# Optimization experiments

Hardware: AMD Instinct MI355X
Metric: run time of the kernel (lower is better)

## Reference

```python
import jax, jax.numpy as jnp
import numpy as np

N = 100000   # num nodes
E = 1600000  # num edges
D = 128      # input_dim
K = 5        # APPNP propagation steps
EPS = 1e-8   # torch cosine_similarity eps


def setup_inputs() -> dict:
    key = jax.random.key(0)
    k1, k2, k3, k4 = jax.random.split(key, 4)
    x = jax.random.normal(k1, (N, D), jnp.float32)
    mask = jax.random.normal(k2, (N, 1), jnp.float32)
    edge_index = jax.random.randint(k3, (2, E), 0, N, dtype=jnp.int32)
    # init_t: orthogonal weight with gain sqrt(2), zero bias
    W = jax.nn.initializers.orthogonal(scale=2 ** 0.5)(k4, (D, D), jnp.float32)
    b = jnp.zeros((D,), jnp.float32)
    alpha = jnp.array(0.5, jnp.float32)
    return {"x": x, "mask": mask, "edge_index": edge_index, "W": W, "b": b, "alpha": alpha}


def reference(x, mask, edge_index, W, b, alpha):
    n = x.shape[0]
    # x_fn: Linear + Tanh
    h = jnp.tanh(x @ W.T + b)
    src, dst = edge_index[0], edge_index[1]
    hs, hd = h[src], h[dst]  # [E, D] gathers
    # torch F.cosine_similarity with eps-clamped norms
    dot = jnp.sum(hs * hd, axis=-1)
    ns = jnp.maximum(jnp.sqrt(jnp.sum(hs * hs, axis=-1)), EPS)
    nd = jnp.maximum(jnp.sqrt(jnp.sum(hd * hd, axis=-1)), EPS)
    edge_weights = jax.nn.relu(dot / (ns * nd))  # [E]

    fill = jax.nn.relu(mask)  # [N, 1]

    # PyG APPNP: gcn_norm with self loops (fill value 1.0)
    loops = jnp.arange(n, dtype=src.dtype)
    row = jnp.concatenate([src, loops])
    col = jnp.concatenate([dst, loops])
    w = jnp.concatenate([edge_weights, jnp.ones((n,), edge_weights.dtype)])
    deg = jax.ops.segment_sum(w, col, num_segments=n)
    dinv = jnp.where(deg > 0, jax.lax.rsqrt(jnp.maximum(deg, EPS)), 0.0)
    norm = dinv[row] * w * dinv[col]  # [E+N]

    # K-step APPNP: z <- (1-alpha) * A_hat z + alpha * fill
    z = fill
    for _ in range(K):
        agg = jax.ops.segment_sum(norm[:, None] * z[row], col, num_segments=n)
        z = (1.0 - alpha) * agg + alpha * fill
    return z, edge_weights
```

## Files before the change

kernel.cpp:

```cpp
#include <hip/hip_runtime.h>
#include <hip/hip_bf16.h>

typedef __attribute__((ext_vector_type(2))) float f32x2;
typedef __attribute__((ext_vector_type(4))) float f32x4;
typedef __attribute__((ext_vector_type(8))) short short8;

#define D 128
#define EPS 1e-8f
#define BSH 8
#define BSZ 256
#define SMAX 8000
#define OSH 12
#define OBK 4096

__device__ __forceinline__ unsigned int pkbf(float lo, float hi) {
    unsigned int r;
    asm("v_cvt_pk_bf16_f32 %0, %1, %2" : "=v"(r) : "v"(lo), "v"(hi));
    return r;
}

__device__ __forceinline__ float ftanh(float y) {
    float e = __builtin_amdgcn_exp2f(y * 2.885390082f);
    float r = __builtin_amdgcn_rcpf(e + 1.0f);
    return __builtin_fmaf(-2.0f, r, 1.0f);
}

__device__ __forceinline__ int dot4(unsigned int a, unsigned int b, int c) {
#if __has_builtin(__builtin_amdgcn_sdot4)
    return __builtin_amdgcn_sdot4((int)a, (int)b, c, false);
#else
    int r = c;
    r += (int)(char)(a) * (int)(char)(b);
    r += (int)(char)(a >> 8) * (int)(char)(b >> 8);
    r += (int)(char)(a >> 16) * (int)(char)(b >> 16);
    r += (int)(char)(a >> 24) * (int)(char)(b >> 24);
    return r;
#endif
}

__global__ __launch_bounds__(256) void k1_gemm_aux(const float* __restrict__ x,
                                                   const float* __restrict__ W,
                                                   const float* __restrict__ b,
                                                   signed char* __restrict__ hn8,
                                                   int N,
                                                   const float* __restrict__ mask,
                                                   float* __restrict__ fill,
                                                   const int* __restrict__ dst,
                                                   int* __restrict__ M,
                                                   int E, int nbk, int nblk, int chunk,
                                                   int gemmNB) {
    __shared__ char Wlds[D * D * 2];
    int tid = threadIdx.x;

    if (blockIdx.x >= gemmNB) {
        int baux = blockIdx.x - gemmNB;
        int* cnt = (int*)Wlds;
        for (int k = tid; k < nbk; k += 256) cnt[k] = 0;
        int fi = baux * 256 + tid;
        if (fi < N) fill[fi] = fmaxf(mask[fi], 0.0f);
        __syncthreads();
        int beg = baux * chunk, end = min(E, beg + chunk);
        for (int e = beg + tid; e < end; e += 256)
            atomicAdd(&cnt[dst[e] >> BSH], 1);
        __syncthreads();
        for (int k = tid; k < nbk; k += 256)
            M[k * nblk + baux] = cnt[k];
        return;
    }

#pragma unroll
    for (int c = 0; c < 8; ++c) {
        int i = c * 256 + tid;
        float4 lo = *(const float4*)(W + i * 8);
        float4 hi = *(const float4*)(W + i * 8 + 4);
        uint4 v;
        v.x = pkbf(lo.x, lo.y); v.y = pkbf(lo.z, lo.w);
        v.z = pkbf(hi.x, hi.y); v.w = pkbf(hi.z, hi.w);
        int byte = i << 4;
        int swz  = byte ^ (((byte >> 8) & 15) << 4);
        *(uint4*)(Wlds + swz) = v;
    }
    __syncthreads();

    int wave = tid >> 6;
    int lane = tid & 63;
    int l16  = lane & 15;
    int g    = lane >> 4;
    int r0   = blockIdx.x * 64 + wave * 16;

    int arow = r0 + l16;
    if (arow >= N) arow = N - 1;
    union { uint4 u; short8 s; } afr[4];
    const float* xp = x + (size_t)arow * D + g * 8;
#pragma unroll
    for (int kc = 0; kc < 4; ++kc) {
        float4 lo = *(const float4*)(xp + kc * 32);
        float4 hi = *(const float4*)(xp + kc * 32 + 4);
        afr[kc].u.x = pkbf(lo.x, lo.y);
        afr[kc].u.y = pkbf(lo.z, lo.w);
        afr[kc].u.z = pkbf(hi.x, hi.y);
        afr[kc].u.w = pkbf(hi.z, hi.w);
    }

    float bj[8];
#pragma unroll
    for (int j = 0; j < 8; ++j) bj[j] = b[j * 16 + l16];

    f32x4 acc[8];
#pragma unroll
    for (int j = 0; j < 8; ++j) acc[j] = (f32x4){0.f, 0.f, 0.f, 0.f};

#pragma unroll
    for (int j = 0; j < 8; ++j) {
#pragma unroll
        for (int kc = 0; kc < 4; ++kc) {
            int addr = (j * 16 + l16) * 256 + kc * 64 + g * 16;
            const short8* bp = (const short8*)(Wlds + (addr ^ (l16 << 4)));
            acc[j] = __builtin_amdgcn_mfma_f32_16x16x32_bf16(afr[kc].s, *bp, acc[j], 0, 0, 0);
        }
    }

    float sq[4] = {0.f, 0.f, 0.f, 0.f};
#pragma unroll
    for (int j = 0; j < 8; ++j) {
#pragma unroll
        for (int r = 0; r < 4; ++r) {
            float tt = ftanh(acc[j][r] + bj[j]);
            acc[j][r] = tt;
            sq[r] = __builtin_fmaf(tt, tt, sq[r]);
        }
    }
#pragma unroll
    for (int m = 1; m <= 8; m <<= 1) {
#pragma unroll
        for (int r = 0; r < 4; ++r) sq[r] += __shfl_xor(sq[r], m);
    }
#pragma unroll
    for (int r = 0; r < 4; ++r) {
        float inv = rsqrtf(fmaxf(sq[r], 1e-16f)) * 127.0f;
        int row = r0 + g * 4 + r;
        if (row < N) {
#pragma unroll
            for (int j = 0; j < 8; ++j) {
                hn8[(size_t)row * D + j * 16 + l16] =
                    (signed char)__float2int_rn(acc[j][r] * inv);
            }
        }
    }
}

__global__ __launch_bounds__(1024) void scan_blk(const int* __restrict__ cnt,
                                                 int* __restrict__ rp,
                                                 int* __restrict__ bsum, int nq) {
    __shared__ int wsum[16];
    __shared__ int sexcl[16];
    int tid = threadIdx.x, lane = tid & 63, wv = tid >> 6;
    int idx = blockIdx.x * 1024 + tid;
    int4 c = (idx < nq) ? ((const int4*)cnt)[idx] : make_int4(0, 0, 0, 0);
    int tsum = c.x + c.y + c.z + c.w;
    int incl = tsum;
#pragma unroll
    for (int m = 1; m < 64; m <<= 1) {
        int t = __shfl_up(incl, m);
        if (lane >= m) incl += t;
    }
    if (lane == 63) wsum[wv] = incl;
    __syncthreads();
    if (tid == 0) {
        int acc = 0;
#pragma unroll
        for (int k = 0; k < 16; ++k) { int t = wsum[k]; sexcl[k] = acc; acc += t; }
        bsum[blockIdx.x] = acc;
    }
    __syncthreads();
    int excl = sexcl[wv] + incl - tsum;
    if (idx < nq) {
        int4 r;
        r.x = excl; r.y = excl + c.x; r.z = r.y + c.y; r.w = r.z + c.z;
        ((int4*)rp)[idx] = r;
    }
}

__global__ __launch_bounds__(256) void scan_top(int* __restrict__ bsum,
                                                int* __restrict__ boff, int nbs,
                                                int* __restrict__ gcur, int nbk2) {
    for (int k = threadIdx.x; k < nbk2; k += 256) gcur[k] = k << OSH;
    if (threadIdx.x == 0) {
        int acc = 0;
        for (int k = 0; k < nbs; ++k) { int t = bsum[k]; boff[k] = acc; acc += t; }
    }
}

__global__ __launch_bounds__(256) void scan_add(int* __restrict__ data,
                                                const int* __restrict__ boff, int nq) {
    int idx = blockIdx.x * 256 + threadIdx.x;
    if (idx < nq) {
        int off = boff[idx >> 10];
        int4 r = ((int4*)data)[idx];
        r.x += off; r.y += off; r.z += off; r.w += off;
        ((int4*)data)[idx] = r;
    }
}

__global__ __launch_bounds__(256) void bscat_kernel(const int* __restrict__ src,
                                                    const int* __restrict__ dst,
                                                    const int* __restrict__ Mo,
                                                    int2* __restrict__ ebuf,
                                                    int E, int nbk, int nblk, int chunk) {
    extern __shared__ int cur[];
    int b = blockIdx.x;
    for (int k = threadIdx.x; k < nbk; k += 256) cur[k] = Mo[k * nblk + b];
    __syncthreads();
    int beg = b * chunk, end = min(E, beg + chunk);
    for (int e = beg + threadIdx.x; e < end; e += 256) {
        int d = dst[e];
        int k = d >> BSH;
        int p = atomicAdd(&cur[k], 1);
        ebuf[p] = make_int2(src[e], (e << BSH) | (d & (BSZ - 1)));
    }
}

__global__ __launch_bounds__(256) void binsort_kernel(const int* __restrict__ Mo,
                                                      const int2* __restrict__ ebuf,
                                                      int* __restrict__ esrc,
                                                      int* __restrict__ eorig,
                                                      int* __restrict__ rp,
                                                      int E, int N, int nbk, int nblk) {
    extern __shared__ char smem[];
    int2* stage = (int2*)smem;
    int*  cnt   = (int*)(smem + SMAX * 8);
    int k = blockIdx.x;
    int base = Mo[k * nblk];
    int endb = (k + 1 < nbk) ? Mo[(k + 1) * nblk] : E;
    int m = endb - base;
    if (m > SMAX) m = SMAX;

    if (threadIdx.x < BSZ) cnt[threadIdx.x] = 0;
    __syncthreads();
    for (int i = threadIdx.x; i < m; i += 256) {
        int2 v = ebuf[base + i];
        stage[i] = v;
        atomicAdd(&cnt[v.y & (BSZ - 1)], 1);
    }
    __syncthreads();
    if (threadIdx.x == 0) {
        int acc = 0;
#pragma unroll 8
        for (int t = 0; t < BSZ; ++t) { int c = cnt[t]; cnt[t] = acc; acc += c; }
    }
    __syncthreads();
    {
        int node = (k << BSH) + threadIdx.x;
        if (threadIdx.x < BSZ && node < N) rp[node] = base + cnt[threadIdx.x];
        if (k == nbk - 1 && threadIdx.x == 0) rp[N] = E;
    }
    __syncthreads();
    for (int i = threadIdx.x; i < m; i += 256) {
        int2 v = stage[i];
        int p = atomicAdd(&cnt[v.y & (BSZ - 1)], 1);
        esrc[base + p]  = v.x;
        eorig[base + p] = v.y >> BSH;
    }
}

__global__ __launch_bounds__(256) void weight_kernel(const int* __restrict__ rp,
                                                     const int* __restrict__ esrc,
                                                     const signed char* __restrict__ hn8,
                                                     float* __restrict__ warr,
                                                     float* __restrict__ dinv, int N) {
    const float SC = 1.0f / 16129.0f;
    int gid = (blockIdx.x * 256 + threadIdx.x) >> 3;
    int l   = threadIdx.x & 7;
    if (gid >= N) return;
    const uint4* hp = (const uint4*)hn8;
    uint4 dv = hp[(size_t)gid * 8 + l];
    int beg = rp[gid], end = rp[gid + 1];
    float sum = 0.f;
    int s = beg;
    for (; s + 3 < end; s += 4) {
        int i0 = esrc[s], i1 = esrc[s + 1], i2 = esrc[s + 2], i3 = esrc[s + 3];
        uint4 u0 = hp[(size_t)i0 * 8 + l];
        uint4 u1 = hp[(size_t)i1 * 8 + l];
        uint4 u2 = hp[(size_t)i2 * 8 + l];
        uint4 u3 = hp[(size_t)i3 * 8 + l];
        int d0 = dot4(u0.x, dv.x, 0); d0 = dot4(u0.y, dv.y, d0);
        d0 = dot4(u0.z, dv.z, d0);    d0 = dot4(u0.w, dv.w, d0);
        int d1 = dot4(u1.x, dv.x, 0); d1 = dot4(u1.y, dv.y, d1);
        d1 = dot4(u1.z, dv.z, d1);    d1 = dot4(u1.w, dv.w, d1);
        int d2 = dot4(u2.x, dv.x, 0); d2 = dot4(u2.y, dv.y, d2);
        d2 = dot4(u2.z, dv.z, d2);    d2 = dot4(u2.w, dv.w, d2);
        int d3 = dot4(u3.x, dv.x, 0); d3 = dot4(u3.y, dv.y, d3);
        d3 = dot4(u3.z, dv.z, d3);    d3 = dot4(u3.w, dv.w, d3);
#pragma unroll
        for (int m = 4; m >= 1; m >>= 1) {
            d0 += __shfl_xor(d0, m); d1 += __shfl_xor(d1, m);
            d2 += __shfl_xor(d2, m); d3 += __shfl_xor(d3, m);
        }
        float w0 = fmaxf((float)d0 * SC, 0.f), w1 = fmaxf((float)d1 * SC, 0.f);
        float w2 = fmaxf((float)d2 * SC, 0.f), w3 = fmaxf((float)d3 * SC, 0.f);
        if (l == 0) { warr[s] = w0; warr[s + 1] = w1; warr[s + 2] = w2; warr[s + 3] = w3; }
        sum += (w0 + w1) + (w2 + w3);
    }
    for (; s < end; ++s) {
        int i0 = esrc[s];
        uint4 u0 = hp[(size_t)i0 * 8 + l];
        int d0 = dot4(u0.x, dv.x, 0); d0 = dot4(u0.y, dv.y, d0);
        d0 = dot4(u0.z, dv.z, d0);    d0 = dot4(u0.w, dv.w, d0);
#pragma unroll
        for (int m = 4; m >= 1; m >>= 1) d0 += __shfl_xor(d0, m);
        float w0 = fmaxf((float)d0 * SC, 0.f);
        if (l == 0) warr[s] = w0;
        sum += w0;
    }
    if (l == 0) dinv[gid] = rsqrtf(1.0f + sum);
}

__global__ __launch_bounds__(256) void k6_dscat_appnp1(const int* __restrict__ eorig,
                                                       const float* __restrict__ warr,
                                                       int* __restrict__ gcur,
                                                       int2* __restrict__ pbuf,
                                                       int E, int nbk2, int chunk,
                                                       int dscatNB,
                                                       const int* __restrict__ rp,
                                                       const int* __restrict__ esrc,
                                                       float* __restrict__ wfin,
                                                       const float* __restrict__ dinv,
                                                       const float* __restrict__ fill,
                                                       const float* __restrict__ alpha,
                                                       float* __restrict__ zout, int N) {
    if (blockIdx.x < dscatNB) {
        extern __shared__ char smem[];
        int2* stage = (int2*)smem;
        int*  hist  = (int*)(smem + (size_t)chunk * 8);
        int*  lcur  = hist + nbk2;
        int b = blockIdx.x;
        for (int k = threadIdx.x; k < nbk2; k += 256) hist[k] = 0;
        __syncthreads();
        int beg = b * chunk, end = min(E, beg + chunk), m = end - beg;
        for (int i = threadIdx.x; i < m; i += 256) {
            int o = eorig[beg + i];
            float w = warr[beg + i];
            stage[i] = make_int2(o, __float_as_int(w));
            atomicAdd(&hist[o >> OSH], 1);
        }
        __syncthreads();
        for (int k = threadIdx.x; k < nbk2; k += 256) {
            int c = hist[k];
            lcur[k] = c ? atomicAdd(&gcur[k], c) : 0;
        }
        __syncthreads();
        for (int i = threadIdx.x; i < m; i += 256) {
            int2 v = stage[i];
            int p = atomicAdd(&lcur[v.x >> OSH], 1);
            pbuf[p] = v;
        }
        return;
    }
    int t = (blockIdx.x - dscatNB) * 256 + threadIdx.x;
    int i = t >> 2, l = t & 3;
    if (i >= N) return;
    int beg = rp[i], end = rp[i + 1];
    float al = alpha[0];
    float oma = 1.0f - al;
    float di = dinv[i];
    float s = 0.f;
    for (int j = beg + l; j < end; j += 4) {
        int sr = esrc[j];
        float wf = oma * warr[j] * di * dinv[sr];
        wfin[j] = wf;
        s += wf * fill[sr];
    }
    s += __shfl_xor(s, 1);
    s += __shfl_xor(s, 2);
    if (l == 0) {
        float fi = fill[i];
        zout[i] = al * fi + oma * di * di * fi + s;
    }
}

__global__ __launch_bounds__(256) void k7_appnp2_dfin(const int* __restrict__ rp,
                                                      const int* __restrict__ esrc,
                                                      const float* __restrict__ wfin,
                                                      const float* __restrict__ dinv,
                                                      const float* __restrict__ fill,
                                                      const float* __restrict__ zin,
                                                      const float* __restrict__ alpha,
                                                      float* __restrict__ zout, int N,
                                                      int appnpNB,
                                                      const int2* __restrict__ pbuf,
                                                      float* __restrict__ ew, int E) {
    if (blockIdx.x >= appnpNB) {
        int bk = blockIdx.x - appnpNB;
        int base = bk << OSH;
        int m = min(OBK, E - base);
        for (int t = threadIdx.x; t < m; t += 256) {
            int2 v = pbuf[base + t];
            ew[v.x] = __int_as_float(v.y);
        }
        return;
    }
    int t = blockIdx.x * 256 + threadIdx.x;
    int i = t >> 2, l = t & 3;
    if (i >= N) return;
    int beg = rp[i], end = rp[i + 1];
    float s = 0.f;
    for (int j = beg + l; j < end; j += 4)
        s += wfin[j] * zin[esrc[j]];
    s += __shfl_xor(s, 1);
    s += __shfl_xor(s, 2);
    if (l == 0) {
        float al = alpha[0];
        float di = dinv[i];
        zout[i] = al * fill[i] + (1.0f - al) * di * di * zin[i] + s;
    }
}

__global__ __launch_bounds__(256) void appnp_kernel(const int* __restrict__ rp,
                                                    const int* __restrict__ esrc,
                                                    const float* __restrict__ wfin,
                                                    const float* __restrict__ dinv,
                                                    const float* __restrict__ fill,
                                                    const float* __restrict__ zin,
                                                    const float* __restrict__ alpha,
                                                    float* __restrict__ zout, int N) {
    int t = blockIdx.x * 256 + threadIdx.x;
    int i = t >> 2, l = t & 3;
    if (i >= N) return;
    int beg = rp[i], end = rp[i + 1];
    float s = 0.f;
    for (int j = beg + l; j < end; j += 4)
        s += wfin[j] * zin[esrc[j]];
    s += __shfl_xor(s, 1);
    s += __shfl_xor(s, 2);
    if (l == 0) {
        float al = alpha[0];
        float di = dinv[i];
        zout[i] = al * fill[i] + (1.0f - al) * di * di * zin[i] + s;
    }
}

extern "C" void kernel_launch(void* const* d_in, const int* in_sizes, int n_in,
                              void* d_out, int out_size, void* d_ws, size_t ws_size,
                              hipStream_t stream) {
    const float* x     = (const float*)d_in[0];
    const float* mask  = (const float*)d_in[1];
    const int*   ei    = (const int*)d_in[2];
    const float* W     = (const float*)d_in[3];
    const float* b     = (const float*)d_in[4];
    const float* alpha = (const float*)d_in[5];

    int N = in_sizes[1];
    int E = in_sizes[2] / 2;
    const int* src = ei;
    const int* dst = ei + E;

    float* out = (float*)d_out;
    float* ew  = out + N;

    int Np = (N + 15) & ~15;

    int NBK  = (N + BSZ - 1) >> BSH;
    int NBLK = 400;
    int CHUNK = (E + NBLK - 1) / NBLK;
    int L = NBK * NBLK;

    int NBK2   = (E + OBK - 1) >> OSH;
    int NBLK2  = 400;
    int CHUNK2 = (E + NBLK2 - 1) / NBLK2;

    int GEMM_NB = (N + 63) / 64;
    int nb_n4   = ((size_t)N * 4 + 255) / 256;

    char* wsb = (char*)d_ws;
    signed char* hn8 = (signed char*)wsb;
    int2* pbuf = (int2*)wsb;
    char* p = wsb + (size_t)N * D;
    float* dinv = (float*)p;           p += (size_t)Np * 4;
    float* fill = (float*)p;           p += (size_t)Np * 4;
    float* zA   = (float*)p;           p += (size_t)Np * 4;
    float* zB   = (float*)p;           p += (size_t)Np * 4;
    int*   rp   = (int*)p;             p += (size_t)(Np + 16) * 4;
    int*   M    = (int*)p;             p += (size_t)L * 4;
    int*   Mo   = (int*)p;             p += (size_t)(L + 16) * 4;
    int*   bsum = (int*)p;             p += 64 * 4;
    int*   boff = (int*)p;             p += 64 * 4;
    int*   gcur = (int*)p;             p += 512 * 4;
    int2*  ebuf = (int2*)p;            p += (size_t)E * 8;
    int*   esrc = (int*)p;             p += (size_t)E * 4;
    int*   eorig= (int*)p;             p += (size_t)E * 4;
    float* warr = (float*)p;           p += (size_t)E * 4;
    float* wfin = (float*)p;

    int nq   = L / 4;
    int nbs  = (nq + 1023) / 1024;
    int ldsA = ((NBK * 4) + 15) & ~15;
    int ldsB = SMAX * 8 + BSZ * 4;
    int ldsD = CHUNK2 * 8 + 2 * NBK2 * 4;

    k1_gemm_aux<<<GEMM_NB + NBLK, 256, 0, stream>>>(x, W, b, hn8, N, mask, fill,
                                                    dst, M, E, NBK, NBLK, CHUNK, GEMM_NB);
    scan_blk<<<nbs, 1024, 0, stream>>>(M, Mo, bsum, nq);
    scan_top<<<1, 256, 0, stream>>>(bsum, boff, nbs, gcur, NBK2);
    scan_add<<<(nq + 255) / 256, 256, 0, stream>>>(Mo, boff, nq);
    bscat_kernel<<<NBLK, 256, ldsA, stream>>>(src, dst, Mo, ebuf, E, NBK, NBLK, CHUNK);
    binsort_kernel<<<NBK, 256, ldsB, stream>>>(Mo, ebuf, esrc, eorig, rp, E, N, NBK, NBLK);

    weight_kernel<<<((size_t)N * 8 + 255) / 256, 256, 0, stream>>>(rp, esrc, hn8, warr, dinv, N);

    k6_dscat_appnp1<<<NBLK2 + nb_n4, 256, ldsD, stream>>>(eorig, warr, gcur, pbuf,
                                                          E, NBK2, CHUNK2, NBLK2,
                                                          rp, esrc, wfin, dinv, fill,
                                                          alpha, zA, N);
    k7_appnp2_dfin<<<nb_n4 + NBK2, 256, 0, stream>>>(rp, esrc, wfin, dinv, fill,
                                                     zA, alpha, zB, N, nb_n4,
                                                     pbuf, ew, E);

    appnp_kernel<<<nb_n4, 256, 0, stream>>>(rp, esrc, wfin, dinv, fill, zB, alpha, zA, N);
    appnp_kernel<<<nb_n4, 256, 0, stream>>>(rp, esrc, wfin, dinv, fill, zA, alpha, zB, N);
    appnp_kernel<<<nb_n4, 256, 0, stream>>>(rp, esrc, wfin, dinv, fill, zB, alpha, out, N);
}
```

Before: 199.8 us.

## Pack edge src/weight pairs, fold scan_add into consumers, widen GEMM and weight loops

Several changes at once. The GEMM kernel now processes two 16-row tiles per wave, which halves the block count and amortizes the W staging in LDS. The scan_add launch is removed, and bscat and binsort add the block offset (boff) when they read Mo. The weight kernel unrolls its gather to 8 edges per iteration to put more loads in flight. The APPNP kernels read an interleaved int2 (src, weight) array so each edge costs one load instead of two. The workspace layout must now fit an int2 array where a float array was, which raises the workspace requirement.

```diff
diff --git a/kernel.cpp b/kernel.cpp
--- a/kernel.cpp
+++ b/kernel.cpp
@@ -86,64 +86,65 @@
     int lane = tid & 63;
     int l16  = lane & 15;
     int g    = lane >> 4;
-    int r0   = blockIdx.x * 64 + wave * 16;
-
-    int arow = r0 + l16;
-    if (arow >= N) arow = N - 1;
-    union { uint4 u; short8 s; } afr[4];
-    const float* xp = x + (size_t)arow * D + g * 8;
-#pragma unroll
-    for (int kc = 0; kc < 4; ++kc) {
-        float4 lo = *(const float4*)(xp + kc * 32);
-        float4 hi = *(const float4*)(xp + kc * 32 + 4);
-        afr[kc].u.x = pkbf(lo.x, lo.y);
-        afr[kc].u.y = pkbf(lo.z, lo.w);
-        afr[kc].u.z = pkbf(hi.x, hi.y);
-        afr[kc].u.w = pkbf(hi.z, hi.w);
-    }
 
     float bj[8];
 #pragma unroll
     for (int j = 0; j < 8; ++j) bj[j] = b[j * 16 + l16];
 
-    f32x4 acc[8];
-#pragma unroll
-    for (int j = 0; j < 8; ++j) acc[j] = (f32x4){0.f, 0.f, 0.f, 0.f};
-
-#pragma unroll
-    for (int j = 0; j < 8; ++j) {
+    for (int tt = 0; tt < 2; ++tt) {
+        int r0 = blockIdx.x * 128 + wave * 32 + tt * 16;
+        int arow = r0 + l16;
+        if (arow >= N) arow = N - 1;
+        union { uint4 u; short8 s; } afr[4];
+        const float* xp = x + (size_t)arow * D + g * 8;
 #pragma unroll
         for (int kc = 0; kc < 4; ++kc) {
-            int addr = (j * 16 + l16) * 256 + kc * 64 + g * 16;
-            const short8* bp = (const short8*)(Wlds + (addr ^ (l16 << 4)));
-            acc[j] = __builtin_amdgcn_mfma_f32_16x16x32_bf16(afr[kc].s, *bp, acc[j], 0, 0, 0);
-        }
-    }
-
-    float sq[4] = {0.f, 0.f, 0.f, 0.f};
-#pragma unroll
-    for (int j = 0; j < 8; ++j) {
+            float4 lo = *(const float4*)(xp + kc * 32);
+            float4 hi = *(const float4*)(xp + kc * 32 + 4);
+            afr[kc].u.x = pkbf(lo.x, lo.y);
+            afr[kc].u.y = pkbf(lo.z, lo.w);
+            afr[kc].u.z = pkbf(hi.x, hi.y);
+            afr[kc].u.w = pkbf(hi.z, hi.w);
+        }
+
+        f32x4 acc[8];
+#pragma unroll
+        for (int j = 0; j < 8; ++j) acc[j] = (f32x4){0.f, 0.f, 0.f, 0.f};
+#pragma unroll
+        for (int j = 0; j < 8; ++j) {
+#pragma unroll
+            for (int kc = 0; kc < 4; ++kc) {
+                int addr = (j * 16 + l16) * 256 + kc * 64 + g * 16;
+                const short8* bp = (const short8*)(Wlds + (addr ^ (l16 << 4)));
+                acc[j] = __builtin_amdgcn_mfma_f32_16x16x32_bf16(afr[kc].s, *bp, acc[j], 0, 0, 0);
+            }
+        }
+
+        float sq[4] = {0.f, 0.f, 0.f, 0.f};
+#pragma unroll
+        for (int j = 0; j < 8; ++j) {
+#pragma unroll
+            for (int r = 0; r < 4; ++r) {
+                float tv = ftanh(acc[j][r] + bj[j]);
+                acc[j][r] = tv;
+                sq[r] = __builtin_fmaf(tv, tv, sq[r]);
+            }
+        }
+#pragma unroll
+        for (int m = 1; m <= 8; m <<= 1) {
+#pragma unroll
+            for (int r = 0; r < 4; ++r) sq[r] += __shfl_xor(sq[r], m);
+        }
 #pragma unroll
         for (int r = 0; r < 4; ++r) {
-            float tt = ftanh(acc[j][r] + bj[j]);
-            acc[j][r] = tt;
-            sq[r] = __builtin_fmaf(tt, tt, sq[r]);
-        }
-    }
-#pragma unroll
-    for (int m = 1; m <= 8; m <<= 1) {
-#pragma unroll
-        for (int r = 0; r < 4; ++r) sq[r] += __shfl_xor(sq[r], m);
-    }
-#pragma unroll
-    for (int r = 0; r < 4; ++r) {
-        float inv = rsqrtf(fmaxf(sq[r], 1e-16f)) * 127.0f;
-        int row = r0 + g * 4 + r;
-        if (row < N) {
-#pragma unroll
-            for (int j = 0; j < 8; ++j) {
-                hn8[(size_t)row * D + j * 16 + l16] =
-                    (signed char)__float2int_rn(acc[j][r] * inv);
+            float inv = rsqrtf(fmaxf(sq[r], 1e-16f)) * 127.0f;
+            int row = r0 + g * 4 + r;
+            if (row < N) {
+#pragma unroll
+                for (int j = 0; j < 8; ++j) {
+                    hn8[(size_t)row * D + j * 16 + l16] =
+                        (signed char)__float2int_rn(acc[j][r] * inv);
+                }
             }
         }
     }
@@ -191,25 +192,18 @@
     }
 }
 
-__global__ __launch_bounds__(256) void scan_add(int* __restrict__ data,
-                                                const int* __restrict__ boff, int nq) {
-    int idx = blockIdx.x * 256 + threadIdx.x;
-    if (idx < nq) {
-        int off = boff[idx >> 10];
-        int4 r = ((int4*)data)[idx];
-        r.x += off; r.y += off; r.z += off; r.w += off;
-        ((int4*)data)[idx] = r;
-    }
-}
-
 __global__ __launch_bounds__(256) void bscat_kernel(const int* __restrict__ src,
                                                     const int* __restrict__ dst,
                                                     const int* __restrict__ Mo,
+                                                    const int* __restrict__ boff,
                                                     int2* __restrict__ ebuf,
                                                     int E, int nbk, int nblk, int chunk) {
     extern __shared__ int cur[];
     int b = blockIdx.x;
-    for (int k = threadIdx.x; k < nbk; k += 256) cur[k] = Mo[k * nblk + b];
+    for (int k = threadIdx.x; k < nbk; k += 256) {
+        int e = k * nblk + b;
+        cur[k] = Mo[e] + boff[e >> 12];
+    }
     __syncthreads();
     int beg = b * chunk, end = min(E, beg + chunk);
     for (int e = beg + threadIdx.x; e < end; e += 256) {
@@ -221,6 +215,7 @@
 }
 
 __global__ __launch_bounds__(256) void binsort_kernel(const int* __restrict__ Mo,
+                                                      const int* __restrict__ boff,
                                                       const int2* __restrict__ ebuf,
                                                       int* __restrict__ esrc,
                                                       int* __restrict__ eorig,
@@ -230,8 +225,13 @@
     int2* stage = (int2*)smem;
     int*  cnt   = (int*)(smem + SMAX * 8);
     int k = blockIdx.x;
-    int base = Mo[k * nblk];
-    int endb = (k + 1 < nbk) ? Mo[(k + 1) * nblk] : E;
+    int eb = k * nblk;
+    int base = Mo[eb] + boff[eb >> 12];
+    int endb = E;
+    if (k + 1 < nbk) {
+        int e2 = (k + 1) * nblk;
+        endb = Mo[e2] + boff[e2 >> 12];
+    }
     int m = endb - base;
     if (m > SMAX) m = SMAX;
 
@@ -277,33 +277,35 @@
     int beg = rp[gid], end = rp[gid + 1];
     float sum = 0.f;
     int s = beg;
-    for (; s + 3 < end; s += 4) {
-        int i0 = esrc[s], i1 = esrc[s + 1], i2 = esrc[s + 2], i3 = esrc[s + 3];
-        uint4 u0 = hp[(size_t)i0 * 8 + l];
-        uint4 u1 = hp[(size_t)i1 * 8 + l];
-        uint4 u2 = hp[(size_t)i2 * 8 + l];
-        uint4 u3 = hp[(size_t)i3 * 8 + l];
-        int d0 = dot4(u0.x, dv.x, 0); d0 = dot4(u0.y, dv.y, d0);
-        d0 = dot4(u0.z, dv.z, d0);    d0 = dot4(u0.w, dv.w, d0);
-        int d1 = dot4(u1.x, dv.x, 0); d1 = dot4(u1.y, dv.y, d1);
-        d1 = dot4(u1.z, dv.z, d1);    d1 = dot4(u1.w, dv.w, d1);
-        int d2 = dot4(u2.x, dv.x, 0); d2 = dot4(u2.y, dv.y, d2);
-        d2 = dot4(u2.z, dv.z, d2);    d2 = dot4(u2.w, dv.w, d2);
-        int d3 = dot4(u3.x, dv.x, 0); d3 = dot4(u3.y, dv.y, d3);
-        d3 = dot4(u3.z, dv.z, d3);    d3 = dot4(u3.w, dv.w, d3);
+    for (; s + 7 < end; s += 8) {
+        uint4 u[8];
+        int dd[8];
+#pragma unroll
+        for (int q = 0; q < 8; ++q) u[q] = hp[(size_t)esrc[s + q] * 8 + l];
+#pragma unroll
+        for (int q = 0; q < 8; ++q) {
+            int d0 = dot4(u[q].x, dv.x, 0); d0 = dot4(u[q].y, dv.y, d0);
+            d0 = dot4(u[q].z, dv.z, d0);    d0 = dot4(u[q].w, dv.w, d0);
+            dd[q] = d0;
+        }
 #pragma unroll
         for (int m = 4; m >= 1; m >>= 1) {
-            d0 += __shfl_xor(d0, m); d1 += __shfl_xor(d1, m);
-            d2 += __shfl_xor(d2, m); d3 += __shfl_xor(d3, m);
-        }
-        float w0 = fmaxf((float)d0 * SC, 0.f), w1 = fmaxf((float)d1 * SC, 0.f);
-        float w2 = fmaxf((float)d2 * SC, 0.f), w3 = fmaxf((float)d3 * SC, 0.f);
-        if (l == 0) { warr[s] = w0; warr[s + 1] = w1; warr[s + 2] = w2; warr[s + 3] = w3; }
-        sum += (w0 + w1) + (w2 + w3);
+#pragma unroll
+            for (int q = 0; q < 8; ++q) dd[q] += __shfl_xor(dd[q], m);
+        }
+        float wv[8];
+#pragma unroll
+        for (int q = 0; q < 8; ++q) {
+            wv[q] = fmaxf((float)dd[q] * SC, 0.f);
+            sum += wv[q];
+        }
+        if (l == 0) {
+#pragma unroll
+            for (int q = 0; q < 8; ++q) warr[s + q] = wv[q];
+        }
     }
     for (; s < end; ++s) {
-        int i0 = esrc[s];
-        uint4 u0 = hp[(size_t)i0 * 8 + l];
+        uint4 u0 = hp[(size_t)esrc[s] * 8 + l];
         int d0 = dot4(u0.x, dv.x, 0); d0 = dot4(u0.y, dv.y, d0);
         d0 = dot4(u0.z, dv.z, d0);    d0 = dot4(u0.w, dv.w, d0);
 #pragma unroll
@@ -323,7 +325,7 @@
                                                        int dscatNB,
                                                        const int* __restrict__ rp,
                                                        const int* __restrict__ esrc,
-                                                       float* __restrict__ wfin,
+                                                       int2* __restrict__ pw,
                                                        const float* __restrict__ dinv,
                                                        const float* __restrict__ fill,
                                                        const float* __restrict__ alpha,
@@ -367,7 +369,7 @@
     for (int j = beg + l; j < end; j += 4) {
         int sr = esrc[j];
         float wf = oma * warr[j] * di * dinv[sr];
-        wfin[j] = wf;
+        pw[j] = make_int2(sr, __float_as_int(wf));
         s += wf * fill[sr];
     }
     s += __shfl_xor(s, 1);
@@ -379,8 +381,7 @@
 }
 
 __global__ __launch_bounds__(256) void k7_appnp2_dfin(const int* __restrict__ rp,
-                                                      const int* __restrict__ esrc,
-                                                      const float* __restrict__ wfin,
+                                                      const int2* __restrict__ pw,
                                                       const float* __restrict__ dinv,
                                                       const float* __restrict__ fill,
                                                       const float* __restrict__ zin,
@@ -404,8 +405,10 @@
     if (i >= N) return;
     int beg = rp[i], end = rp[i + 1];
     float s = 0.f;
-    for (int j = beg + l; j < end; j += 4)
-        s += wfin[j] * zin[esrc[j]];
+    for (int j = beg + l; j < end; j += 4) {
+        int2 p = pw[j];
+        s += __int_as_float(p.y) * zin[p.x];
+    }
     s += __shfl_xor(s, 1);
     s += __shfl_xor(s, 2);
     if (l == 0) {
@@ -416,8 +419,7 @@
 }
 
 __global__ __launch_bounds__(256) void appnp_kernel(const int* __restrict__ rp,
-                                                    const int* __restrict__ esrc,
-                                                    const float* __restrict__ wfin,
+                                                    const int2* __restrict__ pw,
                                                     const float* __restrict__ dinv,
                                                     const float* __restrict__ fill,
                                                     const float* __restrict__ zin,
@@ -428,8 +430,10 @@
     if (i >= N) return;
     int beg = rp[i], end = rp[i + 1];
     float s = 0.f;
-    for (int j = beg + l; j < end; j += 4)
-        s += wfin[j] * zin[esrc[j]];
+    for (int j = beg + l; j < end; j += 4) {
+        int2 p = pw[j];
+        s += __int_as_float(p.y) * zin[p.x];
+    }
     s += __shfl_xor(s, 1);
     s += __shfl_xor(s, 2);
     if (l == 0) {
@@ -468,7 +472,7 @@
     int NBLK2  = 400;
     int CHUNK2 = (E + NBLK2 - 1) / NBLK2;
 
-    int GEMM_NB = (N + 63) / 64;
+    int GEMM_NB = (N + 127) / 128;
     int nb_n4   = ((size_t)N * 4 + 255) / 256;
 
     char* wsb = (char*)d_ws;
@@ -489,7 +493,7 @@
     int*   esrc = (int*)p;             p += (size_t)E * 4;
     int*   eorig= (int*)p;             p += (size_t)E * 4;
     float* warr = (float*)p;           p += (size_t)E * 4;
-    float* wfin = (float*)p;
+    int2*  pw   = (int2*)p;
 
     int nq   = L / 4;
     int nbs  = (nq + 1023) / 1024;
@@ -501,21 +505,20 @@
                                                     dst, M, E, NBK, NBLK, CHUNK, GEMM_NB);
     scan_blk<<<nbs, 1024, 0, stream>>>(M, Mo, bsum, nq);
     scan_top<<<1, 256, 0, stream>>>(bsum, boff, nbs, gcur, NBK2);
-    scan_add<<<(nq + 255) / 256, 256, 0, stream>>>(Mo, boff, nq);
-    bscat_kernel<<<NBLK, 256, ldsA, stream>>>(src, dst, Mo, ebuf, E, NBK, NBLK, CHUNK);
-    binsort_kernel<<<NBK, 256, ldsB, stream>>>(Mo, ebuf, esrc, eorig, rp, E, N, NBK, NBLK);
+    bscat_kernel<<<NBLK, 256, ldsA, stream>>>(src, dst, Mo, boff, ebuf, E, NBK, NBLK, CHUNK);
+    binsort_kernel<<<NBK, 256, ldsB, stream>>>(Mo, boff, ebuf, esrc, eorig, rp, E, N, NBK, NBLK);
 
     weight_kernel<<<((size_t)N * 8 + 255) / 256, 256, 0, stream>>>(rp, esrc, hn8, warr, dinv, N);
 
     k6_dscat_appnp1<<<NBLK2 + nb_n4, 256, ldsD, stream>>>(eorig, warr, gcur, pbuf,
                                                           E, NBK2, CHUNK2, NBLK2,
-                                                          rp, esrc, wfin, dinv, fill,
+                                                          rp, esrc, pw, dinv, fill,
                                                           alpha, zA, N);
-    k7_appnp2_dfin<<<nb_n4 + NBK2, 256, 0, stream>>>(rp, esrc, wfin, dinv, fill,
+    k7_appnp2_dfin<<<nb_n4 + NBK2, 256, 0, stream>>>(rp, pw, dinv, fill,
                                                      zA, alpha, zB, N, nb_n4,
                                                      pbuf, ew, E);
 
-    appnp_kernel<<<nb_n4, 256, 0, stream>>>(rp, esrc, wfin, dinv, fill, zB, alpha, zA, N);
-    appnp_kernel<<<nb_n4, 256, 0, stream>>>(rp, esrc, wfin, dinv, fill, zA, alpha, zB, N);
-    appnp_kernel<<<nb_n4, 256, 0, stream>>>(rp, esrc, wfin, dinv, fill, zB, alpha, out, N);
-}
+    appnp_kernel<<<nb_n4, 256, 0, stream>>>(rp, pw, dinv, fill, zB, alpha, zA, N);
+    appnp_kernel<<<nb_n4, 256, 0, stream>>>(rp, pw, dinv, fill, zA, alpha, zB, N);
+    appnp_kernel<<<nb_n4, 256, 0, stream>>>(rp, pw, dinv, fill, zB, alpha, out, N);
+}
```

Result: faster. 193.9 us (-2.9%).
